# Optimization experiments

Measured on AMD Instinct MI355X. Metric: run time of the kernel, lower is better.

The kernel has to match this reference:

```python
import jax, jax.numpy as jnp
import numpy as np

B_SZ, SEQ, D_MODEL, N_STATE = 4, 2048, 768, 16


def setup_inputs() -> dict:
    key = jax.random.key(0)
    ks = jax.random.split(key, 8)
    s = 1.0 / np.sqrt(D_MODEL)
    x = jax.random.normal(ks[0], (B_SZ, SEQ, D_MODEL), dtype=jnp.float32)
    W1 = jax.random.uniform(ks[1], (D_MODEL, D_MODEL), jnp.float32, -s, s)
    b1 = jax.random.uniform(ks[2], (D_MODEL,), jnp.float32, -s, s)
    W2 = jax.random.uniform(ks[3], (D_MODEL, N_STATE), jnp.float32, -s, s)
    b2 = jax.random.uniform(ks[4], (N_STATE,), jnp.float32, -s, s)
    W3 = jax.random.uniform(ks[5], (D_MODEL, N_STATE), jnp.float32, -s, s)
    b3 = jax.random.uniform(ks[6], (N_STATE,), jnp.float32, -s, s)
    # A: xavier_uniform over (d_model, state_size)
    a_bound = np.sqrt(6.0 / (D_MODEL + N_STATE))
    A = jax.random.uniform(ks[7], (D_MODEL, N_STATE), jnp.float32, -a_bound, a_bound)
    return {"x": x, "W1": W1, "b1": b1, "W2": W2, "b2": b2, "W3": W3, "b3": b3, "A": A}


def reference(x, W1, b1, W2, b2, W3, b3, A):
    # Input-dependent projections
    Bm = x @ W2 + b2                     # [b, l, n]
    Cm = x @ W3 + b3                     # [b, l, n]
    delta = jax.nn.softplus(x @ W1 + b1)  # [b, l, d]
    # Discretization (S6)
    dB = delta[..., None] * Bm[:, :, None, :]                 # [b, l, d, n]
    dA = jnp.exp(jnp.einsum('bld,dn->bldn', delta, A))        # [b, l, d, n]
    # Source initializes h to zeros, so the dA*h term vanishes (no recurrence).
    h0 = jnp.zeros_like(dB)
    h = dA * h0 + x[..., None] * dB                            # [b, l, d, n]
    y = jnp.einsum('bln,bldn->bld', Cm, h)                     # [b, l, d]
    return y
```

## Files before the change

kernel.cpp:

```cpp
#include <hip/hip_runtime.h>
#include <hip/hip_bf16.h>
#include <math.h>


#define M_ROWS 8192
#define DM 768
#define NS 16

typedef short bf16x8 __attribute__((ext_vector_type(8)));
typedef unsigned short u16x8 __attribute__((ext_vector_type(8)));
typedef float f32x4 __attribute__((ext_vector_type(4)));

__device__ __forceinline__ unsigned short f2bf(float f) {
    union { float f; unsigned u; } v; v.f = f;
    unsigned r = v.u + 0x7FFF + ((v.u >> 16) & 1);
    return (unsigned short)(r >> 16);
}
__device__ __forceinline__ unsigned short cvtbf(float f) {
    __hip_bfloat16 h = __float2bfloat16(f);
    return *reinterpret_cast<unsigned short*>(&h);
}
__device__ __forceinline__ void async16(const void* g, void* l) {
    __builtin_amdgcn_global_load_lds(
        (const __attribute__((address_space(1))) void*)g,
        (__attribute__((address_space(3))) void*)l,
        16, 0, 0);
}
__device__ __forceinline__ float softplus_fast(float v) {
    return fmaxf(v, 0.f) + __logf(1.f + __expf(-fabsf(v)));
}

__global__ __launch_bounds__(256) void prep_kernel(
    const float* __restrict__ W1,
    const float* __restrict__ W2,
    const float* __restrict__ W3,
    unsigned short* __restrict__ w1t,
    unsigned short* __restrict__ w23t)
{
    __shared__ float tile[32][33];
    const int bid = blockIdx.x;
    const int tid = threadIdx.x;
    if (bid < 32) {
        const int n = bid, i = n >> 1;
        const float* src = (n & 1) ? W3 : W2;
        #pragma unroll
        for (int e = 0; e < 3; ++e) {
            int k = e * 256 + tid;
            w23t[n * DM + k] = f2bf(src[k * NS + i]);
        }
    } else {
        const int b2i = bid - 32;
        const int n0 = (b2i % 24) * 32, k0 = (b2i / 24) * 32;
        const int tx = tid & 31, ty = tid >> 5;
        #pragma unroll
        for (int i = 0; i < 4; ++i) {
            int k = ty + i * 8;
            tile[k][tx] = W1[(k0 + k) * DM + n0 + tx];
        }
        __syncthreads();
        #pragma unroll
        for (int i = 0; i < 4; ++i) {
            int n = ty + i * 8;
            w1t[(n0 + n) * DM + k0 + tx] = f2bf(tile[tx][n]);
        }
    }
}

__global__ __launch_bounds__(256) void gemm_fused_kernel(
    const float* __restrict__ x,
    const unsigned short* __restrict__ w1t,
    const unsigned short* __restrict__ w23t,
    const float* __restrict__ b1,
    const float* __restrict__ b2, const float* __restrict__ b3,
    float* __restrict__ y)
{
    __shared__ unsigned short Al[128 * 64];
    __shared__ unsigned short Bl[64 * 64];
    __shared__ unsigned short Wl[32 * 64];
    __shared__ float spart[2][128];
    const int b = blockIdx.x;
    const int c = b & 7, j = b >> 3;
    const int m0 = (c * 8 + j / 12) * 128;
    const int n0 = (j % 12) * 64;
    const int tid  = threadIdx.x;
    const int lane = tid & 63;
    const int wave = tid >> 6;
    const int wm = wave >> 1, wn = wave & 1;
    const int l15 = lane & 15, quad = lane >> 4;

    f32x4 acc[4][2];
    f32x4 accP[4];
    #pragma unroll
    for (int i = 0; i < 4; ++i) {
        accP[i] = (f32x4){0.f, 0.f, 0.f, 0.f};
        #pragma unroll
        for (int jj = 0; jj < 2; ++jj)
            acc[i][jj] = (f32x4){0.f, 0.f, 0.f, 0.f};
    }

    for (int k0 = 0; k0 < DM; k0 += 64) {
        float4 va[8];
        #pragma unroll
        for (int i = 0; i < 4; ++i) {
            int ch = tid + i * 256;
            int r = ch >> 3, jg = (ch & 7) ^ (r & 7);
            const float4* src = (const float4*)(x + (m0 + r) * DM + k0 + jg * 8);
            va[2 * i]     = src[0];
            va[2 * i + 1] = src[1];
        }
        #pragma unroll
        for (int i = 0; i < 2; ++i) {
            int ch = tid + i * 256;
            int r = ch >> 3, jg = (ch & 7) ^ (r & 7);
            async16(w1t + (n0 + r) * DM + k0 + jg * 8, Bl + ch * 8);
        }
        {
            int ch = tid;
            int r = ch >> 3, jg = (ch & 7) ^ (r & 7);
            async16(w23t + r * DM + k0 + jg * 8, Wl + ch * 8);
        }
        #pragma unroll
        for (int i = 0; i < 4; ++i) {
            int ch = tid + i * 256;
            float4 a = va[2 * i], bb = va[2 * i + 1];
            u16x8 o;
            o[0] = cvtbf(a.x);  o[1] = cvtbf(a.y);
            o[2] = cvtbf(a.z);  o[3] = cvtbf(a.w);
            o[4] = cvtbf(bb.x); o[5] = cvtbf(bb.y);
            o[6] = cvtbf(bb.z); o[7] = cvtbf(bb.w);
            *(u16x8*)(Al + ch * 8) = o;
        }
        __syncthreads();

        #pragma unroll
        for (int kk = 0; kk < 2; ++kk) {
            bf16x8 bfr[2], wfr;
            #pragma unroll
            for (int jj = 0; jj < 2; ++jj) {
                int rb = wn * 32 + jj * 16 + l15;
                int jb = (kk * 4 + quad) ^ (rb & 7);
                bfr[jj] = *(const bf16x8*)(Bl + rb * 64 + jb * 8);
            }
            {
                int rw = wn * 16 + l15;
                int jw = (kk * 4 + quad) ^ (rw & 7);
                wfr = *(const bf16x8*)(Wl + rw * 64 + jw * 8);
            }
            #pragma unroll
            for (int i = 0; i < 4; ++i) {
                int rr = wm * 64 + i * 16 + l15;
                int ja = (kk * 4 + quad) ^ (rr & 7);
                bf16x8 af = *(const bf16x8*)(Al + rr * 64 + ja * 8);
                #pragma unroll
                for (int jj = 0; jj < 2; ++jj)
                    acc[i][jj] = __builtin_amdgcn_mfma_f32_16x16x32_bf16(
                        af, bfr[jj], acc[i][jj], 0, 0, 0);
                accP[i] = __builtin_amdgcn_mfma_f32_16x16x32_bf16(
                    af, wfr, accP[i], 0, 0, 0);
            }
        }
        __syncthreads();
    }

    {
        const int p = wn * 8 + (l15 >> 1);
        const float bB = b2[p], bC = b3[p];
        #pragma unroll
        for (int i = 0; i < 4; ++i) {
            float sacc[4];
            #pragma unroll
            for (int r = 0; r < 4; ++r) {
                float v = accP[i][r];
                float pv = __shfl_xor(v, 1, 64);
                sacc[r] = (l15 & 1) ? (pv + bB) * (v + bC)
                                    : (v + bB) * (pv + bC);
                sacc[r] += __shfl_xor(sacc[r], 1, 64);
                sacc[r] += __shfl_xor(sacc[r], 2, 64);
                sacc[r] += __shfl_xor(sacc[r], 4, 64);
                sacc[r] += __shfl_xor(sacc[r], 8, 64);
            }
            if (l15 == 0) {
                #pragma unroll
                for (int r = 0; r < 4; ++r)
                    spart[wn][wm * 64 + i * 16 + quad * 4 + r] = 0.5f * sacc[r];
            }
        }
    }
    __syncthreads();

    #pragma unroll
    for (int i = 0; i < 4; ++i) {
        const int rl = wm * 64 + i * 16 + quad * 4;
        const int rowbase = m0 + rl;
        float sv4[4];
        #pragma unroll
        for (int r = 0; r < 4; ++r)
            sv4[r] = spart[0][rl + r] + spart[1][rl + r];
        #pragma unroll
        for (int jj = 0; jj < 2; ++jj) {
            int gcol = n0 + wn * 32 + jj * 16 + l15;
            float bias = b1[gcol];
            #pragma unroll
            for (int r = 0; r < 4; ++r) {
                int grow = rowbase + r;
                float v = acc[i][jj][r] + bias;
                float sp = softplus_fast(v);
                float xv = x[grow * DM + gcol];
                y[grow * DM + gcol] = xv * sp * sv4[r];
            }
        }
    }
}

extern "C" void kernel_launch(void* const* d_in, const int* in_sizes, int n_in,
                              void* d_out, int out_size, void* d_ws, size_t ws_size,
                              hipStream_t stream) {
    const float* x  = (const float*)d_in[0];
    const float* W1 = (const float*)d_in[1];
    const float* b1 = (const float*)d_in[2];
    const float* W2 = (const float*)d_in[3];
    const float* b2 = (const float*)d_in[4];
    const float* W3 = (const float*)d_in[5];
    const float* b3 = (const float*)d_in[6];
    float* y = (float*)d_out;

    unsigned short* w1t  = (unsigned short*)d_ws;
    unsigned short* w23t = (unsigned short*)((char*)d_ws + 1179648);

    prep_kernel<<<608, 256, 0, stream>>>(W1, W2, W3, w1t, w23t);
    gemm_fused_kernel<<<768, 256, 0, stream>>>(x, w1t, w23t, b1, b2, b3, y);
}
```

Before: 115.7 us.

## Double-buffer GEMM K-loop in LDS and load W23 fragments straight to registers

Restructures the K loop into a fully unrolled, double-buffered pipeline. The x tile for step t+2 is prefetched into registers and the w1t tile is issued asynchronously into the alternate LDS buffer while MFMAs run on the current buffer, leaving one barrier per iteration instead of two. The small W2/W3 fragment is now read directly from global memory into registers and no longer staged in LDS. The costs are doubled LDS for the A and B tiles and higher register pressure from the prefetch registers and full unrolling, which may reduce occupancy.

```diff
diff --git a/kernel.cpp b/kernel.cpp
--- a/kernel.cpp
+++ b/kernel.cpp
@@ -6,6 +6,7 @@
 #define M_ROWS 8192
 #define DM 768
 #define NS 16
+#define NT 12
 
 typedef short bf16x8 __attribute__((ext_vector_type(8)));
 typedef unsigned short u16x8 __attribute__((ext_vector_type(8)));
@@ -74,9 +75,8 @@
     const float* __restrict__ b2, const float* __restrict__ b3,
     float* __restrict__ y)
 {
-    __shared__ unsigned short Al[128 * 64];
-    __shared__ unsigned short Bl[64 * 64];
-    __shared__ unsigned short Wl[32 * 64];
+    __shared__ unsigned short Al[2][128 * 64];
+    __shared__ unsigned short Bl[2][64 * 64];
     __shared__ float spart[2][128];
     const int b = blockIdx.x;
     const int c = b & 7, j = b >> 3;
@@ -98,59 +98,80 @@
             acc[i][jj] = (f32x4){0.f, 0.f, 0.f, 0.f};
     }
 
-    for (int k0 = 0; k0 < DM; k0 += 64) {
-        float4 va[8];
-        #pragma unroll
-        for (int i = 0; i < 4; ++i) {
-            int ch = tid + i * 256;
-            int r = ch >> 3, jg = (ch & 7) ^ (r & 7);
-            const float4* src = (const float4*)(x + (m0 + r) * DM + k0 + jg * 8);
-            va[2 * i]     = src[0];
-            va[2 * i + 1] = src[1];
-        }
-        #pragma unroll
-        for (int i = 0; i < 2; ++i) {
-            int ch = tid + i * 256;
-            int r = ch >> 3, jg = (ch & 7) ^ (r & 7);
-            async16(w1t + (n0 + r) * DM + k0 + jg * 8, Bl + ch * 8);
-        }
-        {
-            int ch = tid;
-            int r = ch >> 3, jg = (ch & 7) ^ (r & 7);
-            async16(w23t + r * DM + k0 + jg * 8, Wl + ch * 8);
-        }
-        #pragma unroll
-        for (int i = 0; i < 4; ++i) {
-            int ch = tid + i * 256;
-            float4 a = va[2 * i], bb = va[2 * i + 1];
-            u16x8 o;
-            o[0] = cvtbf(a.x);  o[1] = cvtbf(a.y);
-            o[2] = cvtbf(a.z);  o[3] = cvtbf(a.w);
-            o[4] = cvtbf(bb.x); o[5] = cvtbf(bb.y);
-            o[6] = cvtbf(bb.z); o[7] = cvtbf(bb.w);
-            *(u16x8*)(Al + ch * 8) = o;
-        }
-        __syncthreads();
-
+    float4 va[8];
+    bf16x8 vw[2][2];
+
+#define LOAD_A(T) do {                                                     \
+        const int k0_ = (T) * 64;                                          \
+        _Pragma("unroll")                                                  \
+        for (int i_ = 0; i_ < 4; ++i_) {                                   \
+            int ch_ = tid + i_ * 256;                                      \
+            int r_ = ch_ >> 3, jg_ = (ch_ & 7) ^ (r_ & 7);                 \
+            const float4* s_ = (const float4*)(x + (m0 + r_) * DM + k0_ + jg_ * 8); \
+            va[2 * i_]     = s_[0];                                        \
+            va[2 * i_ + 1] = s_[1];                                        \
+        }                                                                  \
+    } while (0)
+
+#define LOAD_W(P, T) do {                                                  \
+        const int k0_ = (T) * 64;                                          \
+        const int rw_ = wn * 16 + l15;                                     \
+        _Pragma("unroll")                                                  \
+        for (int kk_ = 0; kk_ < 2; ++kk_)                                  \
+            vw[P][kk_] = *(const bf16x8*)(w23t + rw_ * DM + k0_ + (kk_ * 4 + quad) * 8); \
+    } while (0)
+
+#define STAGE_B(P, T) do {                                                 \
+        const int k0_ = (T) * 64;                                          \
+        _Pragma("unroll")                                                  \
+        for (int i_ = 0; i_ < 2; ++i_) {                                   \
+            int ch_ = tid + i_ * 256;                                      \
+            int r_ = ch_ >> 3, jg_ = (ch_ & 7) ^ (r_ & 7);                 \
+            async16(w1t + (n0 + r_) * DM + k0_ + jg_ * 8, &Bl[P][ch_ * 8]); \
+        }                                                                  \
+    } while (0)
+
+#define CVT_WRITE_A(P) do {                                                \
+        _Pragma("unroll")                                                  \
+        for (int i_ = 0; i_ < 4; ++i_) {                                   \
+            int ch_ = tid + i_ * 256;                                      \
+            float4 a_ = va[2 * i_], b_ = va[2 * i_ + 1];                   \
+            u16x8 o_;                                                      \
+            o_[0] = cvtbf(a_.x); o_[1] = cvtbf(a_.y);                      \
+            o_[2] = cvtbf(a_.z); o_[3] = cvtbf(a_.w);                      \
+            o_[4] = cvtbf(b_.x); o_[5] = cvtbf(b_.y);                      \
+            o_[6] = cvtbf(b_.z); o_[7] = cvtbf(b_.w);                      \
+            *(u16x8*)(&Al[P][ch_ * 8]) = o_;                               \
+        }                                                                  \
+    } while (0)
+
+    LOAD_A(0);
+    LOAD_W(0, 0);
+    STAGE_B(0, 0);
+    CVT_WRITE_A(0);
+    LOAD_A(1);
+    LOAD_W(1, 1);
+    __syncthreads();
+    STAGE_B(1, 1);
+
+    #pragma unroll
+    for (int t = 0; t < NT; ++t) {
+        const int cur = t & 1;
         #pragma unroll
         for (int kk = 0; kk < 2; ++kk) {
-            bf16x8 bfr[2], wfr;
+            bf16x8 bfr[2];
             #pragma unroll
             for (int jj = 0; jj < 2; ++jj) {
                 int rb = wn * 32 + jj * 16 + l15;
                 int jb = (kk * 4 + quad) ^ (rb & 7);
-                bfr[jj] = *(const bf16x8*)(Bl + rb * 64 + jb * 8);
-            }
-            {
-                int rw = wn * 16 + l15;
-                int jw = (kk * 4 + quad) ^ (rw & 7);
-                wfr = *(const bf16x8*)(Wl + rw * 64 + jw * 8);
-            }
+                bfr[jj] = *(const bf16x8*)(&Bl[cur][rb * 64 + jb * 8]);
+            }
+            bf16x8 wfr = vw[cur][kk];
             #pragma unroll
             for (int i = 0; i < 4; ++i) {
                 int rr = wm * 64 + i * 16 + l15;
                 int ja = (kk * 4 + quad) ^ (rr & 7);
-                bf16x8 af = *(const bf16x8*)(Al + rr * 64 + ja * 8);
+                bf16x8 af = *(const bf16x8*)(&Al[cur][rr * 64 + ja * 8]);
                 #pragma unroll
                 for (int jj = 0; jj < 2; ++jj)
                     acc[i][jj] = __builtin_amdgcn_mfma_f32_16x16x32_bf16(
@@ -159,7 +180,15 @@
                     af, wfr, accP[i], 0, 0, 0);
             }
         }
-        __syncthreads();
+        if (t + 1 < NT) {
+            CVT_WRITE_A(cur ^ 1);
+            __syncthreads();
+            if (t + 2 < NT) {
+                LOAD_A(t + 2);
+                LOAD_W(cur, t + 2);
+                STAGE_B(cur, t + 2);
+            }
+        }
     }
 
     {
@@ -210,6 +239,10 @@
             }
         }
     }
+#undef LOAD_A
+#undef LOAD_W
+#undef STAGE_B
+#undef CVT_WRITE_A
 }
 
 extern "C" void kernel_launch(void* const* d_in, const int* in_sizes, int n_in,
```

Result: slower. 120.8 us (+4.4%).
